# Kernel optimization log

Measured on AMD Instinct MI355X. Metric: run time of the kernel, lower is better.

The kernel has to match this reference:

```python
import jax, jax.numpy as jnp
import numpy as np
import math

D_MODEL = 1024
NHEAD = 16
FACTOR = 5


def setup_inputs() -> dict:
    key = jax.random.key(0)
    ks = jax.random.split(key, 9)
    d = D_MODEL
    s = 1.0 / math.sqrt(d)
    x = jax.random.normal(ks[0], (2, 2048, d), dtype=jnp.float32)
    Wq = jax.random.normal(ks[1], (d, d), dtype=jnp.float32) * s
    bq = jnp.zeros((d,), dtype=jnp.float32)
    Wk = jax.random.normal(ks[2], (d, d), dtype=jnp.float32) * s
    bk = jnp.zeros((d,), dtype=jnp.float32)
    Wv = jax.random.normal(ks[3], (d, d), dtype=jnp.float32) * s
    bv = jnp.zeros((d,), dtype=jnp.float32)
    Wo = jax.random.normal(ks[4], (d, d), dtype=jnp.float32) * s
    bo = jnp.zeros((d,), dtype=jnp.float32)
    return {"x": x, "Wq": Wq, "bq": bq, "Wk": Wk, "bk": bk,
            "Wv": Wv, "bv": bv, "Wo": Wo, "bo": bo}


def reference(x, Wq, bq, Wk, bk, Wv, bv, Wo, bo):
    B, L, d_model = x.shape
    H = NHEAD
    D = d_model // H
    # U = min(L, int(factor * log(L)))  (static, L > 1)
    U = min(L, int(FACTOR * math.log(L)))

    def proj(W, b):
        # [B,L,d] -> [B,H,L,D]
        return (x @ W.T + b).reshape(B, L, H, D).transpose(0, 2, 1, 3)

    Q = proj(Wq, bq)
    K = proj(Wk, bk)
    V = proj(Wv, bv)

    scores = jnp.einsum('bhqd,bhkd->bhqk', Q, K) / math.sqrt(D)  # [B,H,L,L]
    top_vals, _ = jax.lax.top_k(scores, U)                       # [B,H,L,U]
    thresh = top_vals[..., -1:]                                  # kth largest per row
    scores = jnp.where(scores < thresh, -jnp.inf, scores)
    attn = jax.nn.softmax(scores, axis=-1)                       # dropout p=0 (eval)
    context = jnp.einsum('bhqk,bhkd->bhqd', attn, V)             # [B,H,L,D]
    context = context.transpose(0, 2, 1, 3).reshape(B, L, d_model)
    return context @ Wo.T + bo
```

## Files before the change

kernel.cpp:

```cpp
#include <hip/hip_runtime.h>
#include <math.h>

#define B_SZ 2
#define L_SEQ 2048
#define NH 16
#define HD 64
#define DM 1024
#define TQ 8
#define DELTA 1.2e-5f
#define CAP 224
#define NCAND 16

__global__ __launch_bounds__(256)
void gemm_nt(const float* __restrict__ A, const float* __restrict__ W,
             const float* __restrict__ bias, float* __restrict__ C,
             int M, int N, int K, int mode)
{
    const int BK = 16;
    __shared__ float As[16][68];
    __shared__ float Bs[16][68];
    int tid = threadIdx.x;
    int bn = blockIdx.x * 64;
    int bm = blockIdx.y * 64;
    int tm = tid >> 4;
    int tn = tid & 15;
    int lrow = tid >> 2;
    int lk4  = (tid & 3) * 4;
    float acc[4][4] = {};

    for (int k0 = 0; k0 < K; k0 += BK) {
        float4 av = *(const float4*)(A + (size_t)(bm + lrow) * K + k0 + lk4);
        float4 bv = *(const float4*)(W + (size_t)(bn + lrow) * K + k0 + lk4);
        As[lk4 + 0][lrow] = av.x; As[lk4 + 1][lrow] = av.y;
        As[lk4 + 2][lrow] = av.z; As[lk4 + 3][lrow] = av.w;
        Bs[lk4 + 0][lrow] = bv.x; Bs[lk4 + 1][lrow] = bv.y;
        Bs[lk4 + 2][lrow] = bv.z; Bs[lk4 + 3][lrow] = bv.w;
        __syncthreads();
        #pragma unroll
        for (int kk = 0; kk < BK; ++kk) {
            float4 a4 = *(const float4*)&As[kk][tm * 4];
            float4 b4 = *(const float4*)&Bs[kk][tn * 4];
            float a[4] = {a4.x, a4.y, a4.z, a4.w};
            float b[4] = {b4.x, b4.y, b4.z, b4.w};
            #pragma unroll
            for (int i = 0; i < 4; ++i)
                #pragma unroll
                for (int j = 0; j < 4; ++j)
                    acc[i][j] += a[i] * b[j];
        }
        __syncthreads();
    }

    #pragma unroll
    for (int i = 0; i < 4; ++i) {
        int r = bm + tm * 4 + i;
        #pragma unroll
        for (int j = 0; j < 4; ++j) {
            int c = bn + tn * 4 + j;
            float v = acc[i][j] + ((mode == 2) ? bias[r] : bias[c]);
            if (mode == 0) {
                int b = r >> 11, l = r & (L_SEQ - 1);
                int h = c >> 6,  d = c & (HD - 1);
                C[(((size_t)(b * NH + h)) * L_SEQ + l) * HD + d] = v;
            } else if (mode == 1) {
                C[(size_t)r * N + c] = v;
            } else {
                int h = r >> 6,  d = r & (HD - 1);
                int b = c >> 11, l = c & (L_SEQ - 1);
                C[(((size_t)(b * NH + h)) * HD + d) * L_SEQ + l] = v;
            }
        }
    }
}

__global__ __launch_bounds__(512, 4)
void attn_topk(const float* __restrict__ Q, const float* __restrict__ KT,
               const float* __restrict__ V, float* __restrict__ ctx, int U)
{
    __shared__ float sc[TQ][L_SEQ];
    __shared__ float qs[TQ][HD];
    __shared__ float lp[TQ][CAP];
    __shared__ short lidx[TQ][CAP];
    __shared__ int   hist[TQ][66];

    int tid = threadIdx.x;
    int nb  = gridDim.x;
    int lb  = (blockIdx.x & 7) * (nb >> 3) + (blockIdx.x >> 3);
    int bh  = lb >> 8;
    int qt  = lb & 255;
    int q0  = qt * TQ;

    const float* KTb = KT + (size_t)bh * HD * L_SEQ;
    const float* Vb  = V  + (size_t)bh * L_SEQ * HD;

    {
        int r = tid >> 6, d = tid & 63;
        qs[r][d] = Q[((size_t)bh * L_SEQ + q0 + r) * HD + d] * 0.125f;
    }
    __syncthreads();

    {
        int k4 = tid * 4;
        float4 acc[TQ];
        #pragma unroll
        for (int r = 0; r < TQ; ++r) acc[r] = make_float4(0.f, 0.f, 0.f, 0.f);
        #pragma unroll 4
        for (int d0 = 0; d0 < HD; d0 += 4) {
            float4 qv[TQ];
            #pragma unroll
            for (int r = 0; r < TQ; ++r) qv[r] = *(const float4*)&qs[r][d0];
            #pragma unroll
            for (int dd = 0; dd < 4; ++dd) {
                float4 kt = *(const float4*)(KTb + (size_t)(d0 + dd) * L_SEQ + k4);
                #pragma unroll
                for (int r = 0; r < TQ; ++r) {
                    float q = (dd == 0) ? qv[r].x : (dd == 1) ? qv[r].y
                            : (dd == 2) ? qv[r].z : qv[r].w;
                    acc[r].x += q * kt.x; acc[r].y += q * kt.y;
                    acc[r].z += q * kt.z; acc[r].w += q * kt.w;
                }
            }
        }
        #pragma unroll
        for (int r = 0; r < TQ; ++r)
            *(float4*)&sc[r][k4] = acc[r];
    }
    __syncthreads();

    int wv   = tid >> 6;
    int lane = tid & 63;

    float f[32];
    #pragma unroll
    for (int i = 0; i < 32; ++i)
        f[i] = sc[wv][lane + 64 * i];

    float lmax = -3.402823466e38f;
    #pragma unroll
    for (int i = 0; i < 32; ++i) lmax = fmaxf(lmax, f[i]);
    float mx = lmax, Aanch = lmax;
    #pragma unroll
    for (int m = 32; m; m >>= 1) {
        mx    = fmaxf(mx,    __shfl_xor(mx,    m));
        Aanch = fminf(Aanch, __shfl_xor(Aanch, m));
    }

    float Ln = Aanch;
    float w  = fmaxf(mx - Aanch, 1e-30f);

    {
        float hinv = 62.0f / w;
        hist[wv][lane] = 0;
        if (lane < 2) hist[wv][64 + lane] = 0;
        #pragma unroll
        for (int i = 0; i < 32; ++i) {
            float g = fminf((f[i] - Ln) * hinv + 1.0f, 64.5f);
            if (g >= 0.5f) atomicAdd(&hist[wv][(int)g], 1);
        }
        int v = hist[wv][lane] + ((lane == 63) ? hist[wv][64] : 0);
        #pragma unroll
        for (int d = 1; d < 64; d <<= 1) {
            int t = __shfl_down(v, d);
            if (lane + d < 64) v += t;
        }
        unsigned long long m2 = __ballot(v >= U);
        int bstar = 63 - __clzll((long long)m2);
        if (bstar < 0) bstar = 0;
        float w62 = w * (1.0f / 62.0f);
        Ln = Ln + (float)(bstar - 1) * w62;
        w  = w62;
    }

    float cf[NCAND];
    int nc = 0;
    #pragma unroll
    for (int i = 0; i < 32; ++i) {
        if (f[i] >= Ln) {
            if (nc < NCAND) cf[nc] = f[i];
            nc++;
        }
    }
    bool ovf = __ballot(nc > NCAND) != 0ull;

    for (int pass = 0; pass < 3; ++pass) {
        float hinv = 62.0f / w;
        hist[wv][lane] = 0;
        if (lane < 2) hist[wv][64 + lane] = 0;
        if (!ovf) {
            int n = nc < NCAND ? nc : NCAND;
            for (int j = 0; j < n; ++j) {
                float g = fminf((cf[j] - Ln) * hinv + 1.0f, 64.5f);
                if (g >= 0.5f) atomicAdd(&hist[wv][(int)g], 1);
            }
        } else {
            #pragma unroll
            for (int i = 0; i < 32; ++i) {
                float g = fminf((f[i] - Ln) * hinv + 1.0f, 64.5f);
                if (g >= 0.5f) atomicAdd(&hist[wv][(int)g], 1);
            }
        }
        int v = hist[wv][lane] + ((lane == 63) ? hist[wv][64] : 0);
        #pragma unroll
        for (int d = 1; d < 64; d <<= 1) {
            int t = __shfl_down(v, d);
            if (lane + d < 64) v += t;
        }
        unsigned long long m2 = __ballot(v >= U);
        int bstar = 63 - __clzll((long long)m2);
        if (bstar < 0) bstar = 0;
        float w62 = w * (1.0f / 62.0f);
        Ln = Ln + (float)(bstar - 1) * w62;
        w  = w62;
    }
    float tlo = Ln - w - DELTA;
    float thi = Ln + 2.0f * w + DELTA;

    int rcnt = 0, ccnt = 0, nl = 0;
    unsigned selbits = 0;
    #pragma unroll
    for (int i = 0; i < 32; ++i) {
        bool hi = f[i] > thi;
        bool in = f[i] >= tlo;
        rcnt += hi ? 1 : 0;
        ccnt += (in && !hi) ? 1 : 0;
        if (in) { selbits |= 1u << i; nl++; }
    }
    int pack = (rcnt << 16) | ccnt;
    #pragma unroll
    for (int m = 32; m; m >>= 1) pack += __shfl_xor(pack, m);
    rcnt = pack >> 16; ccnt = pack & 0xFFFF;
    float wm = (float)(U - rcnt) / (float)ccnt;

    int incl = nl;
    #pragma unroll
    for (int d = 1; d < 64; d <<= 1) {
        int v = __shfl_up(incl, d);
        if (lane >= d) incl += v;
    }
    int total = __shfl(incl, 63);
    int off = incl - nl;

    float psum = 0.f;
    unsigned sb = selbits;
    while (sb) {
        int i = __builtin_ctz(sb);
        sb &= sb - 1;
        float wk = (f[i] > thi) ? 1.f : wm;
        float p  = wk * __expf(f[i] - mx);
        psum += p;
        if (off < CAP) {
            lp[wv][off]   = p;
            lidx[wv][off] = (short)(lane + 64 * i);
        }
        off++;
    }
    #pragma unroll
    for (int m = 32; m; m >>= 1) psum += __shfl_xor(psum, m);
    float inv = 1.f / psum;

    int n = total < CAP ? total : CAP;
    float acc = 0.f;
    for (int i = 0; i < n; ++i) {
        float p = lp[wv][i];
        int   k = lidx[wv][i];
        acc += p * Vb[(size_t)k * HD + lane];
    }
    int b = bh >> 4, h = bh & (NH - 1);
    int q = q0 + wv;
    ctx[(((size_t)(b * L_SEQ + q)) * NH + h) * HD + lane] = acc * inv;
}

extern "C" void kernel_launch(void* const* d_in, const int* in_sizes, int n_in,
                              void* d_out, int out_size, void* d_ws, size_t ws_size,
                              hipStream_t stream)
{
    const float* x  = (const float*)d_in[0];
    const float* Wq = (const float*)d_in[1];
    const float* bq = (const float*)d_in[2];
    const float* Wk = (const float*)d_in[3];
    const float* bk = (const float*)d_in[4];
    const float* Wv = (const float*)d_in[5];
    const float* bv = (const float*)d_in[6];
    const float* Wo = (const float*)d_in[7];
    const float* bo = (const float*)d_in[8];
    float* out = (float*)d_out;

    const int M = B_SZ * L_SEQ;
    const int N = DM;
    const int K = DM;

    size_t per = (size_t)M * DM;
    float* Qw  = (float*)d_ws;
    float* KTw = Qw + per;
    float* Vw  = KTw + per;
    float* Cw  = Vw + per;

    int U = (int)(5.0 * log((double)L_SEQ));
    if (U > L_SEQ) U = L_SEQ;

    dim3 blk(256);

    hipLaunchKernelGGL(gemm_nt, dim3(N / 64, M / 64), blk, 0, stream,
                       x, Wq, bq, Qw, M, N, K, 0);
    hipLaunchKernelGGL(gemm_nt, dim3(M / 64, N / 64), blk, 0, stream,
                       Wk, x, bk, KTw, N, M, K, 2);
    hipLaunchKernelGGL(gemm_nt, dim3(N / 64, M / 64), blk, 0, stream,
                       x, Wv, bv, Vw, M, N, K, 0);

    hipLaunchKernelGGL(attn_topk, dim3(B_SZ * NH * (L_SEQ / TQ)), dim3(512),
                       0, stream, Qw, KTw, Vw, Cw, U);

    hipLaunchKernelGGL(gemm_nt, dim3(N / 64, M / 64), blk, 0, stream,
                       Cw, Wo, bo, out, M, N, K, 1);
}
```

Measured before the change: 1.052 ms.

## Enlarge GEMM tiles to 128x128 with double-buffered shared memory and vector stores

Reworks the projection GEMM so each thread computes an 8x8 micro-tile in a 128x128 block tile. Next-k-tile global loads are issued before the current compute and written into a second shared buffer, removing one barrier per iteration. The epilogue now writes float4 stores. The goal is higher arithmetic intensity and less shared-memory and global traffic, at the cost of more registers, fewer blocks (256 per GEMM), and lower occupancy.

```diff
diff --git a/kernel.cpp b/kernel.cpp
--- a/kernel.cpp
+++ b/kernel.cpp
@@ -16,58 +16,88 @@
              const float* __restrict__ bias, float* __restrict__ C,
              int M, int N, int K, int mode)
 {
-    const int BK = 16;
-    __shared__ float As[16][68];
-    __shared__ float Bs[16][68];
+    __shared__ float As[2][16][132];
+    __shared__ float Bs[2][16][132];
     int tid = threadIdx.x;
-    int bn = blockIdx.x * 64;
-    int bm = blockIdx.y * 64;
-    int tm = tid >> 4;
-    int tn = tid & 15;
-    int lrow = tid >> 2;
-    int lk4  = (tid & 3) * 4;
-    float acc[4][4] = {};
-
-    for (int k0 = 0; k0 < K; k0 += BK) {
-        float4 av = *(const float4*)(A + (size_t)(bm + lrow) * K + k0 + lk4);
-        float4 bv = *(const float4*)(W + (size_t)(bn + lrow) * K + k0 + lk4);
-        As[lk4 + 0][lrow] = av.x; As[lk4 + 1][lrow] = av.y;
-        As[lk4 + 2][lrow] = av.z; As[lk4 + 3][lrow] = av.w;
-        Bs[lk4 + 0][lrow] = bv.x; Bs[lk4 + 1][lrow] = bv.y;
-        Bs[lk4 + 2][lrow] = bv.z; Bs[lk4 + 3][lrow] = bv.w;
-        __syncthreads();
-        #pragma unroll
-        for (int kk = 0; kk < BK; ++kk) {
-            float4 a4 = *(const float4*)&As[kk][tm * 4];
-            float4 b4 = *(const float4*)&Bs[kk][tn * 4];
-            float a[4] = {a4.x, a4.y, a4.z, a4.w};
-            float b[4] = {b4.x, b4.y, b4.z, b4.w};
+    int bn = blockIdx.x * 128;
+    int bm = blockIdx.y * 128;
+    int tm = tid >> 4, tn = tid & 15;
+    int lr = tid >> 1, lk = (tid & 1) * 8;
+
+    const float* Ag = A + (size_t)(bm + lr) * K + lk;
+    const float* Bg = W + (size_t)(bn + lr) * K + lk;
+
+    float acc[8][8] = {};
+
+    float4 a0 = *(const float4*)(Ag + 0);
+    float4 a1 = *(const float4*)(Ag + 4);
+    float4 b0 = *(const float4*)(Bg + 0);
+    float4 b1 = *(const float4*)(Bg + 4);
+    As[0][lk+0][lr]=a0.x; As[0][lk+1][lr]=a0.y; As[0][lk+2][lr]=a0.z; As[0][lk+3][lr]=a0.w;
+    As[0][lk+4][lr]=a1.x; As[0][lk+5][lr]=a1.y; As[0][lk+6][lr]=a1.z; As[0][lk+7][lr]=a1.w;
+    Bs[0][lk+0][lr]=b0.x; Bs[0][lk+1][lr]=b0.y; Bs[0][lk+2][lr]=b0.z; Bs[0][lk+3][lr]=b0.w;
+    Bs[0][lk+4][lr]=b1.x; Bs[0][lk+5][lr]=b1.y; Bs[0][lk+6][lr]=b1.z; Bs[0][lk+7][lr]=b1.w;
+    __syncthreads();
+
+    int cur = 0;
+    for (int k0 = 0; k0 < K; k0 += 16) {
+        bool nxt = (k0 + 16) < K;
+        if (nxt) {
+            a0 = *(const float4*)(Ag + k0 + 16);
+            a1 = *(const float4*)(Ag + k0 + 20);
+            b0 = *(const float4*)(Bg + k0 + 16);
+            b1 = *(const float4*)(Bg + k0 + 20);
+        }
+        #pragma unroll
+        for (int kk = 0; kk < 16; ++kk) {
+            float4 aA = *(const float4*)&As[cur][kk][tm*8];
+            float4 aB = *(const float4*)&As[cur][kk][tm*8+4];
+            float4 bA = *(const float4*)&Bs[cur][kk][tn*8];
+            float4 bB = *(const float4*)&Bs[cur][kk][tn*8+4];
+            float av[8] = {aA.x,aA.y,aA.z,aA.w,aB.x,aB.y,aB.z,aB.w};
+            float bv[8] = {bA.x,bA.y,bA.z,bA.w,bB.x,bB.y,bB.z,bB.w};
             #pragma unroll
-            for (int i = 0; i < 4; ++i)
+            for (int i = 0; i < 8; ++i)
                 #pragma unroll
-                for (int j = 0; j < 4; ++j)
-                    acc[i][j] += a[i] * b[j];
-        }
-        __syncthreads();
-    }
-
-    #pragma unroll
-    for (int i = 0; i < 4; ++i) {
-        int r = bm + tm * 4 + i;
-        #pragma unroll
-        for (int j = 0; j < 4; ++j) {
-            int c = bn + tn * 4 + j;
-            float v = acc[i][j] + ((mode == 2) ? bias[r] : bias[c]);
-            if (mode == 0) {
-                int b = r >> 11, l = r & (L_SEQ - 1);
-                int h = c >> 6,  d = c & (HD - 1);
-                C[(((size_t)(b * NH + h)) * L_SEQ + l) * HD + d] = v;
-            } else if (mode == 1) {
-                C[(size_t)r * N + c] = v;
-            } else {
+                for (int j = 0; j < 8; ++j)
+                    acc[i][j] += av[i] * bv[j];
+        }
+        if (nxt) {
+            int nb = cur ^ 1;
+            As[nb][lk+0][lr]=a0.x; As[nb][lk+1][lr]=a0.y; As[nb][lk+2][lr]=a0.z; As[nb][lk+3][lr]=a0.w;
+            As[nb][lk+4][lr]=a1.x; As[nb][lk+5][lr]=a1.y; As[nb][lk+6][lr]=a1.z; As[nb][lk+7][lr]=a1.w;
+            Bs[nb][lk+0][lr]=b0.x; Bs[nb][lk+1][lr]=b0.y; Bs[nb][lk+2][lr]=b0.z; Bs[nb][lk+3][lr]=b0.w;
+            Bs[nb][lk+4][lr]=b1.x; Bs[nb][lk+5][lr]=b1.y; Bs[nb][lk+6][lr]=b1.z; Bs[nb][lk+7][lr]=b1.w;
+            __syncthreads();
+            cur = nb;
+        }
+    }
+
+    #pragma unroll
+    for (int i = 0; i < 8; ++i) {
+        int r = bm + tm*8 + i;
+        #pragma unroll
+        for (int j4 = 0; j4 < 8; j4 += 4) {
+            int c = bn + tn*8 + j4;
+            float4 v;
+            v.x = acc[i][j4+0]; v.y = acc[i][j4+1];
+            v.z = acc[i][j4+2]; v.w = acc[i][j4+3];
+            if (mode == 2) {
+                float bb = bias[r];
+                v.x += bb; v.y += bb; v.z += bb; v.w += bb;
                 int h = r >> 6,  d = r & (HD - 1);
                 int b = c >> 11, l = c & (L_SEQ - 1);
-                C[(((size_t)(b * NH + h)) * HD + d) * L_SEQ + l] = v;
+                *(float4*)&C[(((size_t)(b * NH + h)) * HD + d) * L_SEQ + l] = v;
+            } else {
+                float4 bb = *(const float4*)&bias[c];
+                v.x += bb.x; v.y += bb.y; v.z += bb.z; v.w += bb.w;
+                if (mode == 0) {
+                    int b = r >> 11, l = r & (L_SEQ - 1);
+                    int h = c >> 6,  d = c & (HD - 1);
+                    *(float4*)&C[(((size_t)(b * NH + h)) * L_SEQ + l) * HD + d] = v;
+                } else {
+                    *(float4*)&C[(size_t)r * N + c] = v;
+                }
             }
         }
     }
@@ -300,16 +330,16 @@
 
     dim3 blk(256);
 
-    hipLaunchKernelGGL(gemm_nt, dim3(N / 64, M / 64), blk, 0, stream,
+    hipLaunchKernelGGL(gemm_nt, dim3(N / 128, M / 128), blk, 0, stream,
                        x, Wq, bq, Qw, M, N, K, 0);
-    hipLaunchKernelGGL(gemm_nt, dim3(M / 64, N / 64), blk, 0, stream,
+    hipLaunchKernelGGL(gemm_nt, dim3(M / 128, N / 128), blk, 0, stream,
                        Wk, x, bk, KTw, N, M, K, 2);
-    hipLaunchKernelGGL(gemm_nt, dim3(N / 64, M / 64), blk, 0, stream,
+    hipLaunchKernelGGL(gemm_nt, dim3(N / 128, M / 128), blk, 0, stream,
                        x, Wv, bv, Vw, M, N, K, 0);
 
     hipLaunchKernelGGL(attn_topk, dim3(B_SZ * NH * (L_SEQ / TQ)), dim3(512),
                        0, stream, Qw, KTw, Vw, Cw, U);
 
-    hipLaunchKernelGGL(gemm_nt, dim3(N / 64, M / 64), blk, 0, stream,
+    hipLaunchKernelGGL(gemm_nt, dim3(N / 128, M / 128), blk, 0, stream,
                        Cw, Wo, bo, out, M, N, K, 1);
 }
```

New measurement: 989.9 us. 1.06x faster.
